# Optimization experiments

Hardware: AMD Instinct MI355X
Metric: run time of the kernel (lower is better)

The kernel has to match this reference:

```python
import jax, jax.numpy as jnp
import numpy as np

INPUT_DIM, HIDDEN_DIM, N_CLASSES = 512, 256, 2
TOP_RATIO, MIN_PATCHES, K_INST = 0.7, 128, 8
B, N = 4, 16384


def setup_inputs() -> dict:
    key = jax.random.key(0)
    ks = jax.random.split(key, 10)
    D, H, C = INPUT_DIM, HIDDEN_DIM, N_CLASSES
    s = lambda fan: 1.0 / np.sqrt(fan)
    return {
        "features": jax.random.normal(ks[0], (B, N, D), dtype=jnp.float32),
        # attention_net: Linear(D->H) (dropout is identity in eval)
        "Wa": jax.random.uniform(ks[1], (D, H), minval=-s(D), maxval=s(D), dtype=jnp.float32),
        "ba": jax.random.uniform(ks[2], (H,), minval=-s(D), maxval=s(D), dtype=jnp.float32),
        # per-class attention branches: Linear(H->1), stacked over classes
        "Wbr": jax.random.uniform(ks[3], (C, H), minval=-s(H), maxval=s(H), dtype=jnp.float32),
        "bbr": jax.random.uniform(ks[4], (C,), minval=-s(H), maxval=s(H), dtype=jnp.float32),
        # per-class instance classifiers: Linear(D->H) -> ReLU -> Linear(H->2)
        "W1": jax.random.uniform(ks[5], (C, D, H), minval=-s(D), maxval=s(D), dtype=jnp.float32),
        "b1": jax.random.uniform(ks[6], (C, H), minval=-s(D), maxval=s(D), dtype=jnp.float32),
        "W2": jax.random.uniform(ks[7], (C, H, 2), minval=-s(H), maxval=s(H), dtype=jnp.float32),
        "b2": jax.random.uniform(ks[8], (C, 2), minval=-s(H), maxval=s(H), dtype=jnp.float32),
    }


def reference(features, Wa, ba, Wbr, bbr, W1, b1, W2, b2):
    Bb, Nn, D = features.shape
    C = Wbr.shape[0]

    # ---- compute_attention ----
    h = jax.nn.relu(features @ Wa + ba)                       # (B,N,H)
    a_logits = jnp.einsum('bnh,ch->bcn', h, Wbr) + bbr[None, :, None]
    attn_all = jax.nn.softmax(a_logits, axis=-1)              # (B,C,N)
    combined = attn_all.mean(axis=1)                          # (B,N)

    # ---- per-sample top-k selection (k static under jit) ----
    k = min(max(int(Nn * TOP_RATIO), MIN_PATCHES), Nn)
    _, sel_idx = jax.lax.top_k(combined, k)                   # (B,k)
    sel_idx = jnp.sort(sel_idx, axis=-1)
    selected = jnp.take_along_axis(features, sel_idx[..., None], axis=1)  # (B,k,D)

    # ---- instance clustering loss (vectorized over B x C) ----
    kk = min(K_INST, Nn // 2)
    _, top_idx = jax.lax.top_k(attn_all, kk)                  # (B,C,kk)
    _, bot_idx = jax.lax.top_k(-attn_all, kk)                 # largest=False
    both_idx = jnp.concatenate([top_idx, bot_idx], axis=-1)   # (B,C,2kk)
    inst = features[jnp.arange(Bb)[:, None, None], both_idx]  # (B,C,2kk,D)
    h1 = jax.nn.relu(jnp.einsum('bckd,cdh->bckh', inst, W1) + b1[None, :, None, :])
    logits = jnp.einsum('bckh,cho->bcko', h1, W2) + b2[None, :, None, :]  # (B,C,2kk,2)
    labels = jnp.concatenate([jnp.ones(kk, jnp.int32), jnp.zeros(kk, jnp.int32)])
    logp = jax.nn.log_softmax(logits, axis=-1)
    ce = -jnp.take_along_axis(
        logp, jnp.broadcast_to(labels[None, None, :, None], (Bb, C, 2 * kk, 1)), axis=-1
    )[..., 0]                                                 # (B,C,2kk)
    cl_loss = ce.mean(axis=-1).sum() / (Bb * C)

    return selected, combined, sel_idx, cl_loss
```

## Files before the change

### kernel.cpp

```cpp
#include <hip/hip_runtime.h>

#define NB 4
#define NP 16384
#define DD 512
#define HH 256
#define CC 2
#define KSEL 11468
#define TOTP (NB*NP)
#define BCAP 4096

#define OFF_COMB (NB*KSEL*DD)
#define OFF_IDX  (OFF_COMB + NB*NP)
#define OFF_LOSS (OFF_IDX + NB*KSEL)

#define WS_ALOGIT 0
#define WS_SELIDX (2*NB*CC*NP)
#define WS_MZ     (WS_SELIDX + NB*KSEL)
#define WS_BCNT   (WS_MZ + 16)
#define WS_BLIST  (WS_BCNT + 4)
#define WS_TOP16  (WS_BLIST + NB*BCAP)
#define WS_CE     (WS_TOP16 + 128)
#define WS_CNT    (WS_CE + 128)

typedef __attribute__((ext_vector_type(8))) short short8x;
typedef __attribute__((ext_vector_type(4))) float f32x4;

__device__ __forceinline__ unsigned short f2bf(float x){
  unsigned u = __float_as_uint(x);
  unsigned r = (u + 0x7FFFu + ((u >> 16) & 1u)) >> 16;
  return (unsigned short)r;
}

__device__ __forceinline__ unsigned cvtpk(float lo, float hi){
  unsigned r;
  asm("v_cvt_pk_bf16_f32 %0, %1, %2" : "=v"(r) : "v"(lo), "v"(hi));
  return r;
}

__global__ __launch_bounds__(256) void waconv_kernel(
    const float* __restrict__ Wa, unsigned short* __restrict__ WaT,
    unsigned* __restrict__ donecnt)
{
  __shared__ float tile[32][33];
  const int tx = threadIdx.x, ty = threadIdx.y;
  const int k0 = blockIdx.x * 32, n0 = blockIdx.y * 32;
  if (blockIdx.x==0 && blockIdx.y==0 && tx==0 && ty==0) donecnt[0] = 0u;
  #pragma unroll
  for (int i=0;i<4;++i)
    tile[ty+8*i][tx] = Wa[(size_t)(k0+ty+8*i)*HH + n0 + tx];
  __syncthreads();
  #pragma unroll
  for (int i=0;i<4;++i)
    WaT[(size_t)(n0+ty+8*i)*DD + k0 + tx] = f2bf(tile[tx][ty+8*i]);
}

__global__ __launch_bounds__(512) void gemm_mfma_kernel(
    const float* __restrict__ feat, const unsigned short* __restrict__ WaT,
    const float* __restrict__ ba, const float* __restrict__ Wbr,
    const float* __restrict__ bbr, float* __restrict__ aL)
{
  __shared__ __attribute__((aligned(16))) unsigned char smem[49152];
  __shared__ float sBA[HH], sW0[HH], sW1[HH];
  unsigned char* sA = smem;
  unsigned char* sB = smem + 16384;

  const int tid  = threadIdx.x;
  const int lane = tid & 63;
  const int wid  = tid >> 6;
  const int wm = wid >> 2, wn = wid & 3;
  const int fr = lane & 15, fq = lane >> 4;
  const int p0 = blockIdx.x * 128;
  const float bb0 = bbr[0], bb1 = bbr[1];

  if (tid < HH){ sBA[tid] = ba[tid]; sW0[tid] = Wbr[tid]; sW1[tid] = Wbr[HH+tid]; }

  f32x4 acc[4][4];
  #pragma unroll
  for (int i=0;i<4;++i)
    #pragma unroll
    for (int j=0;j<4;++j)
      acc[i][j] = (f32x4){0.f,0.f,0.f,0.f};

  const int am = tid >> 2, akq = (tid & 3) * 16;
  const int bn = tid >> 1, bhf = tid & 1;

  for (int k0 = 0; k0 < DD; k0 += 64){
    __syncthreads();
    {
      const float4* src = reinterpret_cast<const float4*>(
          feat + (size_t)(p0 + am)*DD + k0 + akq);
      float4 v0 = src[0], v1 = src[1], v2 = src[2], v3 = src[3];
      uint4 w0, w1;
      w0.x = cvtpk(v0.x, v0.y); w0.y = cvtpk(v0.z, v0.w);
      w0.z = cvtpk(v1.x, v1.y); w0.w = cvtpk(v1.z, v1.w);
      w1.x = cvtpk(v2.x, v2.y); w1.y = cvtpk(v2.z, v2.w);
      w1.z = cvtpk(v3.x, v3.y); w1.w = cvtpk(v3.z, v3.w);
      const int swz = (am & 7) << 4;
      *reinterpret_cast<uint4*>(sA + (((am*128) + akq*2) ^ swz)) = w0;
      *reinterpret_cast<uint4*>(sA + (((am*128) + akq*2 + 16) ^ swz)) = w1;
    }
    {
      const uint4* src = reinterpret_cast<const uint4*>(
          WaT + (size_t)bn*DD + k0 + bhf*32);
      uint4 q0 = src[0], q1 = src[1], q2 = src[2], q3 = src[3];
      const int swz = (bn & 7) << 4;
      const int base = bn*128 + bhf*64;
      *reinterpret_cast<uint4*>(sB + ((base     ) ^ swz)) = q0;
      *reinterpret_cast<uint4*>(sB + ((base + 16) ^ swz)) = q1;
      *reinterpret_cast<uint4*>(sB + ((base + 32) ^ swz)) = q2;
      *reinterpret_cast<uint4*>(sB + ((base + 48) ^ swz)) = q3;
    }
    __syncthreads();
    #pragma unroll
    for (int kf = 0; kf < 2; ++kf){
      short8x af[4], bf[4];
      #pragma unroll
      for (int mf = 0; mf < 4; ++mf){
        int m_loc = wm*64 + mf*16 + fr;
        int off = ((m_loc*128 + kf*64 + fq*16) ^ ((m_loc & 7) << 4));
        af[mf] = *reinterpret_cast<const short8x*>(sA + off);
      }
      #pragma unroll
      for (int nf = 0; nf < 4; ++nf){
        int n_loc = wn*64 + nf*16 + fr;
        int off = ((n_loc*128 + kf*64 + fq*16) ^ ((n_loc & 7) << 4));
        bf[nf] = *reinterpret_cast<const short8x*>(sB + off);
      }
      #pragma unroll
      for (int mf = 0; mf < 4; ++mf)
        #pragma unroll
        for (int nf = 0; nf < 4; ++nf)
          acc[mf][nf] = __builtin_amdgcn_mfma_f32_16x16x32_bf16(
              af[mf], bf[nf], acc[mf][nf], 0, 0, 0);
    }
  }
  __syncthreads();

  float* ex = reinterpret_cast<float*>(smem);
  #pragma unroll
  for (int mf = 0; mf < 4; ++mf){
    #pragma unroll
    for (int r = 0; r < 4; ++r){
      float s0 = 0.f, s1 = 0.f;
      #pragma unroll
      for (int nf = 0; nf < 4; ++nf){
        int col = wn*64 + nf*16 + fr;
        float x = fmaxf(acc[mf][nf][r] + sBA[col], 0.f);
        s0 += x * sW0[col];
        s1 += x * sW1[col];
      }
      s0 += __shfl_xor(s0,1); s1 += __shfl_xor(s1,1);
      s0 += __shfl_xor(s0,2); s1 += __shfl_xor(s1,2);
      s0 += __shfl_xor(s0,4); s1 += __shfl_xor(s1,4);
      s0 += __shfl_xor(s0,8); s1 += __shfl_xor(s1,8);
      if (fr == 0){
        int row = wm*64 + mf*16 + fq*4 + r;
        ex[(row*4 + wn)*2 + 0] = s0;
        ex[(row*4 + wn)*2 + 1] = s1;
      }
    }
  }
  __syncthreads();
  if (tid < 256){
    const int row = tid >> 1, c = tid & 1;
    float s = ((ex[(row*4+0)*2+c] + ex[(row*4+1)*2+c]) +
               (ex[(row*4+2)*2+c] + ex[(row*4+3)*2+c]));
    int p = p0 + row;
    int b = p >> 14, nl = p & (NP-1);
    aL[((size_t)b*CC + c)*NP + nl] = s + (c ? bb1 : bb0);
  }
}

__global__ __launch_bounds__(1024) void smstat_kernel(
    const float* __restrict__ aL, float* __restrict__ mz)
{
  __shared__ float  s_redf[16];
  __shared__ double s_redd[16];
  __shared__ float  s_max;
  const int tid = threadIdx.x;
  const int lane = tid & 63, wid = tid >> 6;
  const int r = blockIdx.x;
  const float* a = aL + (size_t)r*NP;
  float m = -1e30f;
  for (int n=tid; n<NP; n+=1024) m = fmaxf(m, a[n]);
  #pragma unroll
  for (int off=1; off<64; off<<=1) m = fmaxf(m, __shfl_xor(m, off));
  if (lane==0) s_redf[wid]=m;
  __syncthreads();
  if (tid==0){ float mm=s_redf[0]; for(int w=1;w<16;++w) mm=fmaxf(mm,s_redf[w]); s_max=mm; }
  __syncthreads();
  m = s_max;
  double ls = 0.0;
  for (int n=tid;n<NP;n+=1024) ls += (double)expf(a[n]-m);
  #pragma unroll
  for (int off=1; off<64; off<<=1) ls += __shfl_xor(ls, off);
  if (lane==0) s_redd[wid]=ls;
  __syncthreads();
  if (tid==0){
    double t=0; for(int w=0;w<16;++w) t+=s_redd[w];
    mz[r*2+0]=m; mz[r*2+1]=(float)(1.0/t);
  }
}

__global__ __launch_bounds__(1024) void selTF_kernel(
    const float* __restrict__ aL, const float* __restrict__ mz,
    float* __restrict__ comb, int* __restrict__ bcnt, int* __restrict__ blist)
{
  __shared__ unsigned s_red[2][16][3];
  __shared__ int s_cnt;
  const int tid = threadIdx.x;
  const int b = blockIdx.x;
  const int lane = tid & 63, wid = tid >> 6;
  const float m0 = mz[b*4+0], iz0 = mz[b*4+1], m1 = mz[b*4+2], iz1 = mz[b*4+3];
  const float* a0 = aL + ((size_t)b*CC + 0)*NP;
  const float* a1 = aL + ((size_t)b*CC + 1)*NP;
  float* oc = comb + (size_t)b*NP;
  const int n0 = tid*16;

  unsigned v[16];
  #pragma unroll
  for (int g=0; g<4; ++g){
    float4 qa = *reinterpret_cast<const float4*>(a0 + n0 + g*4);
    float4 qb = *reinterpret_cast<const float4*>(a1 + n0 + g*4);
    float4 CV;
    CV.x = 0.5f*(expf(qa.x-m0)*iz0 + expf(qb.x-m1)*iz1);
    CV.y = 0.5f*(expf(qa.y-m0)*iz0 + expf(qb.y-m1)*iz1);
    CV.z = 0.5f*(expf(qa.z-m0)*iz0 + expf(qb.z-m1)*iz1);
    CV.w = 0.5f*(expf(qa.w-m0)*iz0 + expf(qb.w-m1)*iz1);
    *reinterpret_cast<float4*>(oc + n0 + g*4) = CV;
    v[g*4+0]=__float_as_uint(CV.x);
    v[g*4+1]=__float_as_uint(CV.y);
    v[g*4+2]=__float_as_uint(CV.z);
    v[g*4+3]=__float_as_uint(CV.w);
  }
  if (tid==0) s_cnt = 0;

  unsigned cur = 0;
  #pragma unroll 1
  for (int bit=30; bit>=12; bit-=2){
    const unsigned t1 = cur | (1u<<bit), t2 = cur | (2u<<bit), t3 = cur | (3u<<bit);
    int c1=0,c2=0,c3=0;
    #pragma unroll
    for (int i=0;i<16;++i){
      c1 += (v[i] >= t1) ? 1 : 0;
      c2 += (v[i] >= t2) ? 1 : 0;
      c3 += (v[i] >= t3) ? 1 : 0;
    }
    #pragma unroll
    for (int off=1; off<64; off<<=1){
      c1+=__shfl_xor(c1,off); c2+=__shfl_xor(c2,off); c3+=__shfl_xor(c3,off);
    }
    const int pb = (bit>>1)&1;
    if (lane==0){ s_red[pb][wid][0]=(unsigned)c1; s_red[pb][wid][1]=(unsigned)c2; s_red[pb][wid][2]=(unsigned)c3; }
    __syncthreads();
    unsigned T1=0,T2=0,T3=0;
    #pragma unroll
    for (int w=0;w<16;++w){ T1+=s_red[pb][w][0]; T2+=s_red[pb][w][1]; T3+=s_red[pb][w][2]; }
    if      (T3 >= KSEL) cur = t3;
    else if (T2 >= KSEL) cur = t2;
    else if (T1 >= KSEL) cur = t1;
  }
  const float Tv = __uint_as_float(cur);
  const float lo = Tv*0.989f, hi = Tv*1.0115f;
  #pragma unroll
  for (int i=0;i<16;++i){
    float x = __uint_as_float(v[i]);
    if (x >= lo && x <= hi){
      int s = atomicAdd(&s_cnt, 1);
      if (s < BCAP) blist[b*BCAP + s] = n0 + i;
    }
  }
  __syncthreads();
  if (tid==0) bcnt[b] = (s_cnt < BCAP) ? s_cnt : BCAP;
}

__global__ __launch_bounds__(512) void recomp_kernel(
    const float* __restrict__ feat, const float* __restrict__ Wa,
    const float* __restrict__ ba, const float* __restrict__ Wbr,
    const float* __restrict__ bbr, const float* __restrict__ mz,
    const int* __restrict__ bcnt, const int* __restrict__ blist,
    float* __restrict__ comb)
{
  __shared__ float fS[16][DD];
  __shared__ float waS[32][HH];
  __shared__ int   s_n[16];
  const int tid = threadIdx.x;
  const int b  = blockIdx.x >> 8;
  const int g0 = (blockIdx.x & 255) * 16;
  const int cnt = bcnt[b];
  if (g0 >= cnt) return;
  if (tid < 16)
    s_n[tid] = (g0 + tid < cnt) ? blist[b*BCAP + g0 + tid] : -1;
  __syncthreads();
  #pragma unroll
  for (int pass=0; pass<4; ++pass){
    const int j = pass*4 + (tid>>7);
    const int c4 = (tid & 127)*4;
    const int n = s_n[j];
    if (n >= 0){
      float4 v = *reinterpret_cast<const float4*>(feat + ((size_t)b*NP + n)*DD + c4);
      *reinterpret_cast<float4*>(&fS[j][c4]) = v;
    }
  }

  const int grp = tid >> 5, l32 = tid & 31;
  const int h0 = l32*4;
  float acc[8];
  #pragma unroll
  for (int i=0;i<8;++i) acc[i]=0.f;

  #pragma unroll 1
  for (int kt=0; kt<16; ++kt){
    __syncthreads();
    {
      const float4* src = reinterpret_cast<const float4*>(Wa + (size_t)(kt*32)*HH);
      float4* dst = reinterpret_cast<float4*>(&waS[0][0]);
      #pragma unroll
      for (int q=0; q<4; ++q) dst[tid + 512*q] = src[tid + 512*q];
    }
    __syncthreads();
    if (s_n[grp] >= 0){
      #pragma unroll
      for (int kk4=0; kk4<8; ++kk4){
        const float4 fv = *reinterpret_cast<const float4*>(&fS[grp][kt*32 + kk4*4]);
        const float fx[4] = {fv.x, fv.y, fv.z, fv.w};
        #pragma unroll
        for (int u=0; u<4; ++u){
          const int kk = kk4*4 + u;
          float4 w0 = *reinterpret_cast<const float4*>(&waS[kk][h0]);
          float4 w1 = *reinterpret_cast<const float4*>(&waS[kk][128 + h0]);
          acc[0] += fx[u]*w0.x; acc[1] += fx[u]*w0.y;
          acc[2] += fx[u]*w0.z; acc[3] += fx[u]*w0.w;
          acc[4] += fx[u]*w1.x; acc[5] += fx[u]*w1.y;
          acc[6] += fx[u]*w1.z; acc[7] += fx[u]*w1.w;
        }
      }
    }
  }
  if (s_n[grp] < 0) return;
  float p0 = 0.f, p1 = 0.f;
  #pragma unroll
  for (int i=0;i<8;++i){
    const int h = (i<4) ? (h0+i) : (128 + h0 + (i-4));
    float x = fmaxf(acc[i] + ba[h], 0.f);
    p0 += x * Wbr[h];
    p1 += x * Wbr[HH+h];
  }
  #pragma unroll
  for (int off=1; off<32; off<<=1){ p0+=__shfl_xor(p0,off); p1+=__shfl_xor(p1,off); }
  if (l32==0){
    const float m0 = mz[b*4+0], iz0 = mz[b*4+1], m1 = mz[b*4+2], iz1 = mz[b*4+3];
    float l0 = p0 + bbr[0];
    float l1 = p1 + bbr[1];
    comb[(size_t)b*NP + s_n[grp]] = 0.5f*(expf(l0-m0)*iz0 + expf(l1-m1)*iz1);
  }
}

__global__ __launch_bounds__(1024) void select_kernel(
    const float* __restrict__ comb, float* __restrict__ outIdxF,
    int* __restrict__ selIdx)
{
  __shared__ unsigned s_red[2][16][3];
  __shared__ unsigned s_wsum[16];
  const int tid = threadIdx.x;
  const int b = blockIdx.x;
  const int lane = tid & 63, wid = tid >> 6;
  const float* row = comb + (size_t)b*NP;

  unsigned v[16];
  {
    const float4* rp = reinterpret_cast<const float4*>(row + tid*16);
    #pragma unroll
    for (int g=0; g<4; ++g){
      float4 q = rp[g];
      v[g*4+0]=__float_as_uint(q.x);
      v[g*4+1]=__float_as_uint(q.y);
      v[g*4+2]=__float_as_uint(q.z);
      v[g*4+3]=__float_as_uint(q.w);
    }
  }
  unsigned cur = 0;
  #pragma unroll 1
  for (int bit=30; bit>=0; bit-=2){
    const unsigned t1 = cur | (1u<<bit), t2 = cur | (2u<<bit), t3 = cur | (3u<<bit);
    int c1=0,c2=0,c3=0;
    #pragma unroll
    for (int i=0;i<16;++i){
      c1 += (v[i] >= t1) ? 1 : 0;
      c2 += (v[i] >= t2) ? 1 : 0;
      c3 += (v[i] >= t3) ? 1 : 0;
    }
    #pragma unroll
    for (int off=1; off<64; off<<=1){
      c1+=__shfl_xor(c1,off); c2+=__shfl_xor(c2,off); c3+=__shfl_xor(c3,off);
    }
    const int pb = (bit>>1)&1;
    if (lane==0){ s_red[pb][wid][0]=(unsigned)c1; s_red[pb][wid][1]=(unsigned)c2; s_red[pb][wid][2]=(unsigned)c3; }
    __syncthreads();
    unsigned T1=0,T2=0,T3=0;
    #pragma unroll
    for (int w=0;w<16;++w){ T1+=s_red[pb][w][0]; T2+=s_red[pb][w][1]; T3+=s_red[pb][w][2]; }
    if      (T3 >= KSEL) cur = t3;
    else if (T2 >= KSEL) cur = t2;
    else if (T1 >= KSEL) cur = t1;
  }
  const unsigned T = cur;
  {
    int c = 0;
    #pragma unroll
    for (int i=0;i<16;++i) c += (v[i] > T) ? 1 : 0;
    #pragma unroll
    for (int off=1; off<64; off<<=1) c += __shfl_xor(c, off);
    if (lane==0) s_red[1][wid][0] = (unsigned)c;
  }
  __syncthreads();
  unsigned gtot=0;
  #pragma unroll
  for (int w=0;w<16;++w) gtot += s_red[1][w][0];
  const int extra = KSEL - (int)gtot;

  int eqc=0;
  #pragma unroll
  for (int i=0;i<16;++i) eqc += (v[i]==T) ? 1 : 0;
  unsigned inc = (unsigned)eqc;
  #pragma unroll
  for (int off=1; off<64; off<<=1){
    unsigned o = __shfl_up(inc, off);
    if (lane >= off) inc += o;
  }
  if (lane==63) s_wsum[wid] = inc;
  __syncthreads();
  unsigned wbase = 0;
  for (int w=0; w<wid; ++w) wbase += s_wsum[w];
  const int eqBase = (int)(wbase + inc) - eqc;

  int eq=eqBase, sc=0;
  #pragma unroll
  for (int i=0;i<16;++i){
    unsigned x = v[i];
    if (x==T){ if (eq<extra) sc++; eq++; }
    else if (x>T) sc++;
  }
  unsigned inc2 = (unsigned)sc;
  #pragma unroll
  for (int off=1; off<64; off<<=1){
    unsigned o = __shfl_up(inc2, off);
    if (lane >= off) inc2 += o;
  }
  __syncthreads();
  if (lane==63) s_wsum[wid] = inc2;
  __syncthreads();
  unsigned wbase2 = 0;
  for (int w=0; w<wid; ++w) wbase2 += s_wsum[w];
  int pos = (int)(wbase2 + inc2) - sc;

  eq=eqBase;
  #pragma unroll
  for (int i=0;i<16;++i){
    unsigned x = v[i];
    int f=0;
    if (x==T){ if (eq<extra) f=1; eq++; }
    else if (x>T) f=1;
    if (f){
      int n = tid*16 + i;
      outIdxF[(size_t)b*KSEL + pos] = (float)n;
      selIdx[(size_t)b*KSEL + pos] = n;
      pos++;
    }
  }
}

__global__ __launch_bounds__(256) void gather_kernel(
    const float* __restrict__ feat, const int* __restrict__ selIdx,
    float* __restrict__ outSel)
{
  const int tid = threadIdx.x;
  const int row = blockIdx.x*2 + (tid>>7);
  const int c4 = tid & 127;
  const int b = row / KSEL;
  const int idx = selIdx[row];
  const float4 v = *reinterpret_cast<const float4*>(feat + ((size_t)b*NP + idx)*DD + c4*4);
  *reinterpret_cast<float4*>(outSel + (size_t)row*DD + c4*4) = v;
}

__global__ __launch_bounds__(256) void top16_kernel(
    const float* __restrict__ aL, const float* __restrict__ mz,
    int* __restrict__ top16)
{
  __shared__ unsigned long long wkT[4][8];
  __shared__ unsigned long long wkB[4][8];
  const int tid = threadIdx.x;
  const int bid = blockIdx.x;
  const int lane = tid & 63, wid = tid >> 6;
  const float* a = aL + (size_t)bid*NP;
  const float m = mz[bid*2+0], iz = mz[bid*2+1];

  unsigned long long t8[8], b8[8];
  #pragma unroll
  for (int i=0;i<8;++i){ t8[i]=0ull; b8[i]=~0ull; }

  for (int j=0;j<16;++j){
    const int n4 = tid + 256*j;
    const float4 v = *reinterpret_cast<const float4*>(a + 4*n4);
    float xs[4];
    xs[0] = expf(v.x-m)*iz; xs[1] = expf(v.y-m)*iz;
    xs[2] = expf(v.z-m)*iz; xs[3] = expf(v.w-m)*iz;
    #pragma unroll
    for (int q=0;q<4;++q){
      const int n = 4*n4 + q;
      const unsigned vb = __float_as_uint(xs[q]);
      unsigned long long kt = ((unsigned long long)vb<<32) | (unsigned)(NP-1-n);
      if (kt > t8[7]){
        t8[7]=kt;
        #pragma unroll
        for (int i=7;i>0;--i){ if (t8[i]>t8[i-1]){ unsigned long long t=t8[i-1]; t8[i-1]=t8[i]; t8[i]=t; } }
      }
      unsigned long long kb = ((unsigned long long)vb<<32) | (unsigned)n;
      if (kb < b8[7]){
        b8[7]=kb;
        #pragma unroll
        for (int i=7;i>0;--i){ if (b8[i]<b8[i-1]){ unsigned long long t=b8[i-1]; b8[i-1]=b8[i]; b8[i]=t; } }
      }
    }
  }

  #pragma unroll
  for (int pick=0; pick<8; ++pick){
    unsigned long long loc = t8[0];
    #pragma unroll
    for (int i=1;i<8;++i) loc = t8[i]>loc ? t8[i] : loc;
    #pragma unroll
    for (int off=1; off<64; off<<=1){ unsigned long long o=__shfl_xor(loc,off); loc=o>loc?o:loc; }
    if (lane==0) wkT[wid][pick]=loc;
    #pragma unroll
    for (int i=0;i<8;++i) if (t8[i]==loc) t8[i]=0ull;
  }
  #pragma unroll
  for (int pick=0; pick<8; ++pick){
    unsigned long long loc = b8[0];
    #pragma unroll
    for (int i=1;i<8;++i) loc = b8[i]<loc ? b8[i] : loc;
    #pragma unroll
    for (int off=1; off<64; off<<=1){ unsigned long long o=__shfl_xor(loc,off); loc=o<loc?o:loc; }
    if (lane==0) wkB[wid][pick]=loc;
    #pragma unroll
    for (int i=0;i<8;++i) if (b8[i]==loc) b8[i]=~0ull;
  }
  __syncthreads();

  if (wid==0){
    unsigned long long k = (lane<32) ? wkT[lane>>3][lane&7] : 0ull;
    #pragma unroll
    for (int pick=0; pick<8; ++pick){
      unsigned long long loc = k;
      #pragma unroll
      for (int off=1; off<64; off<<=1){ unsigned long long o=__shfl_xor(loc,off); loc=o>loc?o:loc; }
      if (k==loc) k=0ull;
      if (lane==0) top16[bid*16+pick] = NP-1-(int)(loc & 0xFFFFFFFFull);
    }
    unsigned long long kb = (lane<32) ? wkB[lane>>3][lane&7] : ~0ull;
    #pragma unroll
    for (int pick=0; pick<8; ++pick){
      unsigned long long loc = kb;
      #pragma unroll
      for (int off=1; off<64; off<<=1){ unsigned long long o=__shfl_xor(loc,off); loc=o<loc?o:loc; }
      if (kb==loc) kb=~0ull;
      if (lane==0) top16[bid*16+8+pick] = (int)(loc & 0xFFFFFFFFull);
    }
  }
}

__global__ __launch_bounds__(256) void mlp_kernel(
    const float* __restrict__ feat, const float* __restrict__ W1,
    const float* __restrict__ b1, const float* __restrict__ W2,
    const float* __restrict__ b2, const int* __restrict__ top16,
    float* __restrict__ cews, unsigned* __restrict__ donecnt,
    float* __restrict__ out_loss)
{
  __shared__ float fS[DD];
  __shared__ float r0[4], r1[4];
  const int tid = threadIdx.x;
  const int bid = blockIdx.x;
  const int r = bid & 15, c = (bid >> 4) & 1, b = bid >> 5;
  const int lane = tid & 63, wid = tid >> 6;
  const int gi = top16[(b*2+c)*16 + r];
  if (tid < 128){
    float4 v = *reinterpret_cast<const float4*>(feat + ((size_t)b*NP + gi)*DD + tid*4);
    *reinterpret_cast<float4*>(&fS[tid*4]) = v;
  }
  __syncthreads();
  const float* w1c = W1 + (size_t)c*DD*HH;
  float a0=0.f,a1=0.f,a2=0.f,a3=0.f;
  #pragma unroll 4
  for (int d=0; d<DD; d+=4){
    a0 += fS[d+0]*w1c[(size_t)(d+0)*HH + tid];
    a1 += fS[d+1]*w1c[(size_t)(d+1)*HH + tid];
    a2 += fS[d+2]*w1c[(size_t)(d+2)*HH + tid];
    a3 += fS[d+3]*w1c[(size_t)(d+3)*HH + tid];
  }
  float h = fmaxf((a0+a1)+(a2+a3) + b1[c*HH+tid], 0.f);
  float p0 = h*W2[(size_t)(c*HH+tid)*2 + 0];
  float p1 = h*W2[(size_t)(c*HH+tid)*2 + 1];
  #pragma unroll
  for (int off=1; off<64; off<<=1){ p0+=__shfl_xor(p0,off); p1+=__shfl_xor(p1,off); }
  if (lane==0){ r0[wid]=p0; r1[wid]=p1; }
  __syncthreads();
  if (tid==0){
    float l0 = (r0[0]+r0[1])+(r0[2]+r0[3]) + b2[c*2+0];
    float l1 = (r1[0]+r1[1])+(r1[2]+r1[3]) + b2[c*2+1];
    float mm = fmaxf(l0,l1);
    float lse = mm + logf(expf(l0-mm)+expf(l1-mm));
    float chosen = (r<8) ? l1 : l0;
    cews[bid] = lse - chosen;
    __threadfence();
    unsigned old = atomicAdd(donecnt, 1u);
    if (old == 127u){
      __threadfence();
      float s=0.f;
      for (int i=0;i<128;++i) s += cews[i];
      out_loss[0] = s / 128.0f;
    }
  }
}

extern "C" void kernel_launch(void* const* d_in, const int* in_sizes, int n_in,
                              void* d_out, int out_size, void* d_ws, size_t ws_size,
                              hipStream_t stream) {
  const float* feat = (const float*)d_in[0];
  const float* Wa   = (const float*)d_in[1];
  const float* ba   = (const float*)d_in[2];
  const float* Wbr  = (const float*)d_in[3];
  const float* bbr  = (const float*)d_in[4];
  const float* W1   = (const float*)d_in[5];
  const float* b1   = (const float*)d_in[6];
  const float* W2   = (const float*)d_in[7];
  const float* b2   = (const float*)d_in[8];
  float* out = (float*)d_out;
  float* ws  = (float*)d_ws;

  float* a_logits = ws + WS_ALOGIT;
  int*   selIdx   = (int*)(ws + WS_SELIDX);
  float* mz       = ws + WS_MZ;
  int*   bcnt     = (int*)(ws + WS_BCNT);
  int*   blist    = (int*)(ws + WS_BLIST);
  int*   top16    = (int*)(ws + WS_TOP16);
  float* cews     = ws + WS_CE;
  unsigned* donecnt = (unsigned*)(ws + WS_CNT);

  unsigned short* WaT = (unsigned short*)d_out;

  hipLaunchKernelGGL(waconv_kernel, dim3(DD/32, HH/32), dim3(32,8), 0, stream,
                     Wa, WaT, donecnt);
  hipLaunchKernelGGL(gemm_mfma_kernel, dim3(TOTP/128), dim3(512), 0, stream,
                     feat, WaT, ba, Wbr, bbr, a_logits);
  hipLaunchKernelGGL(smstat_kernel, dim3(NB*CC), dim3(1024), 0, stream,
                     a_logits, mz);
  hipLaunchKernelGGL(selTF_kernel, dim3(NB), dim3(1024), 0, stream,
                     a_logits, mz, out + OFF_COMB, bcnt, blist);
  hipLaunchKernelGGL(recomp_kernel, dim3(NB*256), dim3(512), 0, stream,
                     feat, Wa, ba, Wbr, bbr, mz, bcnt, blist, out + OFF_COMB);
  hipLaunchKernelGGL(select_kernel, dim3(NB), dim3(1024), 0, stream,
                     out + OFF_COMB, out + OFF_IDX, selIdx);
  hipLaunchKernelGGL(gather_kernel, dim3(NB*KSEL/2), dim3(256), 0, stream,
                     feat, selIdx, out);
  hipLaunchKernelGGL(top16_kernel, dim3(NB*CC), dim3(256), 0, stream,
                     a_logits, mz, top16);
  hipLaunchKernelGGL(mlp_kernel, dim3(NB*CC*16), dim3(256), 0, stream,
                     feat, W1, b1, W2, b2, top16, cews, donecnt, out + OFF_LOSS);
}
```

Measured before the change: 252.0 us.

## Fuse softmax stats, combined-threshold selection and top/bottom-8 into one kernel

Merges the softmax statistics kernel, the combined-attention threshold kernel and the per-class top/bottom-8 kernel into a single kernel with one block per batch sample. Each thread loads its 16 logits for both classes into registers once and reuses them for max, sum, normalised attention, top-k tracking and the radix threshold search. This removes two launches and repeated global reads of the logits. In exchange only 4 blocks do the work that was previously spread over 8+4+8 blocks, and register pressure rises from holding several 16-element arrays per thread.

```diff
diff --git a/kernel.cpp b/kernel.cpp
--- a/kernel.cpp
+++ b/kernel.cpp
@@ -171,80 +171,214 @@
   }
 }
 
-__global__ __launch_bounds__(1024) void smstat_kernel(
-    const float* __restrict__ aL, float* __restrict__ mz)
+__global__ __launch_bounds__(1024) void sel_all_kernel(
+    const float* __restrict__ aL, float* __restrict__ mz,
+    float* __restrict__ comb, int* __restrict__ bcnt,
+    int* __restrict__ blist, int* __restrict__ top16)
 {
-  __shared__ float  s_redf[16];
-  __shared__ double s_redd[16];
-  __shared__ float  s_max;
-  const int tid = threadIdx.x;
-  const int lane = tid & 63, wid = tid >> 6;
-  const int r = blockIdx.x;
-  const float* a = aL + (size_t)r*NP;
-  float m = -1e30f;
-  for (int n=tid; n<NP; n+=1024) m = fmaxf(m, a[n]);
-  #pragma unroll
-  for (int off=1; off<64; off<<=1) m = fmaxf(m, __shfl_xor(m, off));
-  if (lane==0) s_redf[wid]=m;
-  __syncthreads();
-  if (tid==0){ float mm=s_redf[0]; for(int w=1;w<16;++w) mm=fmaxf(mm,s_redf[w]); s_max=mm; }
-  __syncthreads();
-  m = s_max;
-  double ls = 0.0;
-  for (int n=tid;n<NP;n+=1024) ls += (double)expf(a[n]-m);
-  #pragma unroll
-  for (int off=1; off<64; off<<=1) ls += __shfl_xor(ls, off);
-  if (lane==0) s_redd[wid]=ls;
-  __syncthreads();
-  if (tid==0){
-    double t=0; for(int w=0;w<16;++w) t+=s_redd[w];
-    mz[r*2+0]=m; mz[r*2+1]=(float)(1.0/t);
-  }
-}
-
-__global__ __launch_bounds__(1024) void selTF_kernel(
-    const float* __restrict__ aL, const float* __restrict__ mz,
-    float* __restrict__ comb, int* __restrict__ bcnt, int* __restrict__ blist)
-{
+  __shared__ float  s_redf[2][16];
+  __shared__ double s_redd[2][16];
   __shared__ unsigned s_red[2][16][3];
   __shared__ int s_cnt;
+  __shared__ unsigned long long wkT0[16][8], wkB0[16][8];
+  __shared__ unsigned long long wkT1[16][8], wkB1[16][8];
+
   const int tid = threadIdx.x;
   const int b = blockIdx.x;
   const int lane = tid & 63, wid = tid >> 6;
-  const float m0 = mz[b*4+0], iz0 = mz[b*4+1], m1 = mz[b*4+2], iz1 = mz[b*4+3];
   const float* a0 = aL + ((size_t)b*CC + 0)*NP;
   const float* a1 = aL + ((size_t)b*CC + 1)*NP;
-  float* oc = comb + (size_t)b*NP;
   const int n0 = tid*16;
-
-  unsigned v[16];
+  if (tid==0) s_cnt = 0;
+
+  float a0v[16], a1v[16];
   #pragma unroll
   for (int g=0; g<4; ++g){
     float4 qa = *reinterpret_cast<const float4*>(a0 + n0 + g*4);
     float4 qb = *reinterpret_cast<const float4*>(a1 + n0 + g*4);
+    a0v[g*4+0]=qa.x; a0v[g*4+1]=qa.y; a0v[g*4+2]=qa.z; a0v[g*4+3]=qa.w;
+    a1v[g*4+0]=qb.x; a1v[g*4+1]=qb.y; a1v[g*4+2]=qb.z; a1v[g*4+3]=qb.w;
+  }
+
+  float m0l = a0v[0], m1l = a1v[0];
+  #pragma unroll
+  for (int i=1;i<16;++i){ m0l = fmaxf(m0l, a0v[i]); m1l = fmaxf(m1l, a1v[i]); }
+  #pragma unroll
+  for (int off=1; off<64; off<<=1){
+    m0l = fmaxf(m0l, __shfl_xor(m0l, off));
+    m1l = fmaxf(m1l, __shfl_xor(m1l, off));
+  }
+  if (lane==0){ s_redf[0][wid]=m0l; s_redf[1][wid]=m1l; }
+  __syncthreads();
+  float m0 = s_redf[0][0], m1 = s_redf[1][0];
+  #pragma unroll
+  for (int w=1;w<16;++w){ m0 = fmaxf(m0, s_redf[0][w]); m1 = fmaxf(m1, s_redf[1][w]); }
+
+  double ls0 = 0.0, ls1 = 0.0;
+  #pragma unroll
+  for (int i=0;i<16;++i){
+    ls0 += (double)expf(a0v[i]-m0);
+    ls1 += (double)expf(a1v[i]-m1);
+  }
+  #pragma unroll
+  for (int off=1; off<64; off<<=1){ ls0 += __shfl_xor(ls0, off); ls1 += __shfl_xor(ls1, off); }
+  if (lane==0){ s_redd[0][wid]=ls0; s_redd[1][wid]=ls1; }
+  __syncthreads();
+  double t0=0.0, t1=0.0;
+  #pragma unroll
+  for (int w=0;w<16;++w){ t0 += s_redd[0][w]; t1 += s_redd[1][w]; }
+  const float iz0 = (float)(1.0/t0), iz1 = (float)(1.0/t1);
+  if (tid==0){ mz[b*4+0]=m0; mz[b*4+1]=iz0; mz[b*4+2]=m1; mz[b*4+3]=iz1; }
+
+  float e0[16], e1[16];
+  #pragma unroll
+  for (int i=0;i<16;++i){
+    e0[i] = expf(a0v[i]-m0)*iz0;
+    e1[i] = expf(a1v[i]-m1)*iz1;
+  }
+
+  {
+    unsigned long long t8[8], b8[8];
+    #pragma unroll
+    for (int i=0;i<8;++i){ t8[i]=0ull; b8[i]=~0ull; }
+    #pragma unroll
+    for (int i=0;i<16;++i){
+      const int n = n0 + i;
+      const unsigned vb = __float_as_uint(e0[i]);
+      unsigned long long kt = ((unsigned long long)vb<<32) | (unsigned)(NP-1-n);
+      if (kt > t8[7]){
+        t8[7]=kt;
+        #pragma unroll
+        for (int j=7;j>0;--j){ if (t8[j]>t8[j-1]){ unsigned long long t=t8[j-1]; t8[j-1]=t8[j]; t8[j]=t; } }
+      }
+      unsigned long long kb = ((unsigned long long)vb<<32) | (unsigned)n;
+      if (kb < b8[7]){
+        b8[7]=kb;
+        #pragma unroll
+        for (int j=7;j>0;--j){ if (b8[j]<b8[j-1]){ unsigned long long t=b8[j-1]; b8[j-1]=b8[j]; b8[j]=t; } }
+      }
+    }
+    #pragma unroll
+    for (int pick=0; pick<8; ++pick){
+      unsigned long long loc = t8[0];
+      #pragma unroll
+      for (int i=1;i<8;++i) loc = t8[i]>loc ? t8[i] : loc;
+      #pragma unroll
+      for (int off=1; off<64; off<<=1){ unsigned long long o=__shfl_xor(loc,off); loc=o>loc?o:loc; }
+      if (lane==0) wkT0[wid][pick]=loc;
+      #pragma unroll
+      for (int i=0;i<8;++i) if (t8[i]==loc) t8[i]=0ull;
+    }
+    #pragma unroll
+    for (int pick=0; pick<8; ++pick){
+      unsigned long long loc = b8[0];
+      #pragma unroll
+      for (int i=1;i<8;++i) loc = b8[i]<loc ? b8[i] : loc;
+      #pragma unroll
+      for (int off=1; off<64; off<<=1){ unsigned long long o=__shfl_xor(loc,off); loc=o<loc?o:loc; }
+      if (lane==0) wkB0[wid][pick]=loc;
+      #pragma unroll
+      for (int i=0;i<8;++i) if (b8[i]==loc) b8[i]=~0ull;
+    }
+  }
+  {
+    unsigned long long t8[8], b8[8];
+    #pragma unroll
+    for (int i=0;i<8;++i){ t8[i]=0ull; b8[i]=~0ull; }
+    #pragma unroll
+    for (int i=0;i<16;++i){
+      const int n = n0 + i;
+      const unsigned vb = __float_as_uint(e1[i]);
+      unsigned long long kt = ((unsigned long long)vb<<32) | (unsigned)(NP-1-n);
+      if (kt > t8[7]){
+        t8[7]=kt;
+        #pragma unroll
+        for (int j=7;j>0;--j){ if (t8[j]>t8[j-1]){ unsigned long long t=t8[j-1]; t8[j-1]=t8[j]; t8[j]=t; } }
+      }
+      unsigned long long kb = ((unsigned long long)vb<<32) | (unsigned)n;
+      if (kb < b8[7]){
+        b8[7]=kb;
+        #pragma unroll
+        for (int j=7;j>0;--j){ if (b8[j]<b8[j-1]){ unsigned long long t=b8[j-1]; b8[j-1]=b8[j]; b8[j]=t; } }
+      }
+    }
+    #pragma unroll
+    for (int pick=0; pick<8; ++pick){
+      unsigned long long loc = t8[0];
+      #pragma unroll
+      for (int i=1;i<8;++i) loc = t8[i]>loc ? t8[i] : loc;
+      #pragma unroll
+      for (int off=1; off<64; off<<=1){ unsigned long long o=__shfl_xor(loc,off); loc=o>loc?o:loc; }
+      if (lane==0) wkT1[wid][pick]=loc;
+      #pragma unroll
+      for (int i=0;i<8;++i) if (t8[i]==loc) t8[i]=0ull;
+    }
+    #pragma unroll
+    for (int pick=0; pick<8; ++pick){
+      unsigned long long loc = b8[0];
+      #pragma unroll
+      for (int i=1;i<8;++i) loc = b8[i]<loc ? b8[i] : loc;
+      #pragma unroll
+      for (int off=1; off<64; off<<=1){ unsigned long long o=__shfl_xor(loc,off); loc=o<loc?o:loc; }
+      if (lane==0) wkB1[wid][pick]=loc;
+      #pragma unroll
+      for (int i=0;i<8;++i) if (b8[i]==loc) b8[i]=~0ull;
+    }
+  }
+  __syncthreads();
+
+  if (wid==0 || wid==1){
+    unsigned long long (*WT)[8] = (wid==0) ? wkT0 : wkT1;
+    unsigned long long (*WB)[8] = (wid==0) ? wkB0 : wkB1;
+    const int r = b*2 + wid;
+    unsigned long long ka = WT[lane>>2][(lane&3)*2+0];
+    unsigned long long kb = WT[lane>>2][(lane&3)*2+1];
+    #pragma unroll
+    for (int pick=0; pick<8; ++pick){
+      unsigned long long loc = ka>kb ? ka : kb;
+      #pragma unroll
+      for (int off=1; off<64; off<<=1){ unsigned long long o=__shfl_xor(loc,off); loc=o>loc?o:loc; }
+      if (ka==loc) ka=0ull;
+      if (kb==loc) kb=0ull;
+      if (lane==0) top16[r*16+pick] = NP-1-(int)(loc & 0xFFFFFFFFull);
+    }
+    unsigned long long qa = WB[lane>>2][(lane&3)*2+0];
+    unsigned long long qb = WB[lane>>2][(lane&3)*2+1];
+    #pragma unroll
+    for (int pick=0; pick<8; ++pick){
+      unsigned long long loc = qa<qb ? qa : qb;
+      #pragma unroll
+      for (int off=1; off<64; off<<=1){ unsigned long long o=__shfl_xor(loc,off); loc=o<loc?o:loc; }
+      if (qa==loc) qa=~0ull;
+      if (qb==loc) qb=~0ull;
+      if (lane==0) top16[r*16+8+pick] = (int)(loc & 0xFFFFFFFFull);
+    }
+  }
+
+  float cv[16];
+  float* oc = comb + (size_t)b*NP;
+  #pragma unroll
+  for (int g=0; g<4; ++g){
     float4 CV;
-    CV.x = 0.5f*(expf(qa.x-m0)*iz0 + expf(qb.x-m1)*iz1);
-    CV.y = 0.5f*(expf(qa.y-m0)*iz0 + expf(qb.y-m1)*iz1);
-    CV.z = 0.5f*(expf(qa.z-m0)*iz0 + expf(qb.z-m1)*iz1);
-    CV.w = 0.5f*(expf(qa.w-m0)*iz0 + expf(qb.w-m1)*iz1);
+    CV.x = 0.5f*(e0[g*4+0]+e1[g*4+0]);
+    CV.y = 0.5f*(e0[g*4+1]+e1[g*4+1]);
+    CV.z = 0.5f*(e0[g*4+2]+e1[g*4+2]);
+    CV.w = 0.5f*(e0[g*4+3]+e1[g*4+3]);
     *reinterpret_cast<float4*>(oc + n0 + g*4) = CV;
-    v[g*4+0]=__float_as_uint(CV.x);
-    v[g*4+1]=__float_as_uint(CV.y);
-    v[g*4+2]=__float_as_uint(CV.z);
-    v[g*4+3]=__float_as_uint(CV.w);
-  }
-  if (tid==0) s_cnt = 0;
+    cv[g*4+0]=CV.x; cv[g*4+1]=CV.y; cv[g*4+2]=CV.z; cv[g*4+3]=CV.w;
+  }
 
   unsigned cur = 0;
   #pragma unroll 1
   for (int bit=30; bit>=12; bit-=2){
-    const unsigned t1 = cur | (1u<<bit), t2 = cur | (2u<<bit), t3 = cur | (3u<<bit);
+    const unsigned t1u = cur | (1u<<bit), t2u = cur | (2u<<bit), t3u = cur | (3u<<bit);
     int c1=0,c2=0,c3=0;
     #pragma unroll
     for (int i=0;i<16;++i){
-      c1 += (v[i] >= t1) ? 1 : 0;
-      c2 += (v[i] >= t2) ? 1 : 0;
-      c3 += (v[i] >= t3) ? 1 : 0;
+      unsigned x = __float_as_uint(cv[i]);
+      c1 += (x >= t1u) ? 1 : 0;
+      c2 += (x >= t2u) ? 1 : 0;
+      c3 += (x >= t3u) ? 1 : 0;
     }
     #pragma unroll
     for (int off=1; off<64; off<<=1){
@@ -256,15 +390,15 @@
     unsigned T1=0,T2=0,T3=0;
     #pragma unroll
     for (int w=0;w<16;++w){ T1+=s_red[pb][w][0]; T2+=s_red[pb][w][1]; T3+=s_red[pb][w][2]; }
-    if      (T3 >= KSEL) cur = t3;
-    else if (T2 >= KSEL) cur = t2;
-    else if (T1 >= KSEL) cur = t1;
+    if      (T3 >= KSEL) cur = t3u;
+    else if (T2 >= KSEL) cur = t2u;
+    else if (T1 >= KSEL) cur = t1u;
   }
   const float Tv = __uint_as_float(cur);
   const float lo = Tv*0.989f, hi = Tv*1.0115f;
   #pragma unroll
   for (int i=0;i<16;++i){
-    float x = __uint_as_float(v[i]);
+    float x = cv[i];
     if (x >= lo && x <= hi){
       int s = atomicAdd(&s_cnt, 1);
       if (s < BCAP) blist[b*BCAP + s] = n0 + i;
@@ -483,93 +617,6 @@
   *reinterpret_cast<float4*>(outSel + (size_t)row*DD + c4*4) = v;
 }
 
-__global__ __launch_bounds__(256) void top16_kernel(
-    const float* __restrict__ aL, const float* __restrict__ mz,
-    int* __restrict__ top16)
-{
-  __shared__ unsigned long long wkT[4][8];
-  __shared__ unsigned long long wkB[4][8];
-  const int tid = threadIdx.x;
-  const int bid = blockIdx.x;
-  const int lane = tid & 63, wid = tid >> 6;
-  const float* a = aL + (size_t)bid*NP;
-  const float m = mz[bid*2+0], iz = mz[bid*2+1];
-
-  unsigned long long t8[8], b8[8];
-  #pragma unroll
-  for (int i=0;i<8;++i){ t8[i]=0ull; b8[i]=~0ull; }
-
-  for (int j=0;j<16;++j){
-    const int n4 = tid + 256*j;
-    const float4 v = *reinterpret_cast<const float4*>(a + 4*n4);
-    float xs[4];
-    xs[0] = expf(v.x-m)*iz; xs[1] = expf(v.y-m)*iz;
-    xs[2] = expf(v.z-m)*iz; xs[3] = expf(v.w-m)*iz;
-    #pragma unroll
-    for (int q=0;q<4;++q){
-      const int n = 4*n4 + q;
-      const unsigned vb = __float_as_uint(xs[q]);
-      unsigned long long kt = ((unsigned long long)vb<<32) | (unsigned)(NP-1-n);
-      if (kt > t8[7]){
-        t8[7]=kt;
-        #pragma unroll
-        for (int i=7;i>0;--i){ if (t8[i]>t8[i-1]){ unsigned long long t=t8[i-1]; t8[i-1]=t8[i]; t8[i]=t; } }
-      }
-      unsigned long long kb = ((unsigned long long)vb<<32) | (unsigned)n;
-      if (kb < b8[7]){
-        b8[7]=kb;
-        #pragma unroll
-        for (int i=7;i>0;--i){ if (b8[i]<b8[i-1]){ unsigned long long t=b8[i-1]; b8[i-1]=b8[i]; b8[i]=t; } }
-      }
-    }
-  }
-
-  #pragma unroll
-  for (int pick=0; pick<8; ++pick){
-    unsigned long long loc = t8[0];
-    #pragma unroll
-    for (int i=1;i<8;++i) loc = t8[i]>loc ? t8[i] : loc;
-    #pragma unroll
-    for (int off=1; off<64; off<<=1){ unsigned long long o=__shfl_xor(loc,off); loc=o>loc?o:loc; }
-    if (lane==0) wkT[wid][pick]=loc;
-    #pragma unroll
-    for (int i=0;i<8;++i) if (t8[i]==loc) t8[i]=0ull;
-  }
-  #pragma unroll
-  for (int pick=0; pick<8; ++pick){
-    unsigned long long loc = b8[0];
-    #pragma unroll
-    for (int i=1;i<8;++i) loc = b8[i]<loc ? b8[i] : loc;
-    #pragma unroll
-    for (int off=1; off<64; off<<=1){ unsigned long long o=__shfl_xor(loc,off); loc=o<loc?o:loc; }
-    if (lane==0) wkB[wid][pick]=loc;
-    #pragma unroll
-    for (int i=0;i<8;++i) if (b8[i]==loc) b8[i]=~0ull;
-  }
-  __syncthreads();
-
-  if (wid==0){
-    unsigned long long k = (lane<32) ? wkT[lane>>3][lane&7] : 0ull;
-    #pragma unroll
-    for (int pick=0; pick<8; ++pick){
-      unsigned long long loc = k;
-      #pragma unroll
-      for (int off=1; off<64; off<<=1){ unsigned long long o=__shfl_xor(loc,off); loc=o>loc?o:loc; }
-      if (k==loc) k=0ull;
-      if (lane==0) top16[bid*16+pick] = NP-1-(int)(loc & 0xFFFFFFFFull);
-    }
-    unsigned long long kb = (lane<32) ? wkB[lane>>3][lane&7] : ~0ull;
-    #pragma unroll
-    for (int pick=0; pick<8; ++pick){
-      unsigned long long loc = kb;
-      #pragma unroll
-      for (int off=1; off<64; off<<=1){ unsigned long long o=__shfl_xor(loc,off); loc=o<loc?o:loc; }
-      if (kb==loc) kb=~0ull;
-      if (lane==0) top16[bid*16+8+pick] = (int)(loc & 0xFFFFFFFFull);
-    }
-  }
-}
-
 __global__ __launch_bounds__(256) void mlp_kernel(
     const float* __restrict__ feat, const float* __restrict__ W1,
     const float* __restrict__ b1, const float* __restrict__ W2,
@@ -653,18 +700,14 @@
                      Wa, WaT, donecnt);
   hipLaunchKernelGGL(gemm_mfma_kernel, dim3(TOTP/128), dim3(512), 0, stream,
                      feat, WaT, ba, Wbr, bbr, a_logits);
-  hipLaunchKernelGGL(smstat_kernel, dim3(NB*CC), dim3(1024), 0, stream,
-                     a_logits, mz);
-  hipLaunchKernelGGL(selTF_kernel, dim3(NB), dim3(1024), 0, stream,
-                     a_logits, mz, out + OFF_COMB, bcnt, blist);
+  hipLaunchKernelGGL(sel_all_kernel, dim3(NB), dim3(1024), 0, stream,
+                     a_logits, mz, out + OFF_COMB, bcnt, blist, top16);
   hipLaunchKernelGGL(recomp_kernel, dim3(NB*256), dim3(512), 0, stream,
                      feat, Wa, ba, Wbr, bbr, mz, bcnt, blist, out + OFF_COMB);
   hipLaunchKernelGGL(select_kernel, dim3(NB), dim3(1024), 0, stream,
                      out + OFF_COMB, out + OFF_IDX, selIdx);
   hipLaunchKernelGGL(gather_kernel, dim3(NB*KSEL/2), dim3(256), 0, stream,
                      feat, selIdx, out);
-  hipLaunchKernelGGL(top16_kernel, dim3(NB*CC), dim3(256), 0, stream,
-                     a_logits, mz, top16);
   hipLaunchKernelGGL(mlp_kernel, dim3(NB*CC*16), dim3(256), 0, stream,
                      feat, W1, b1, W2, b2, top16, cews, donecnt, out + OFF_LOSS);
 }
```

Measured after the change: 309.1 us. +22.6%, slower.
